# Optimization experiments

Measured on AMD Instinct MI355X. Metric: run time of the kernel, lower is better.

The kernel has to match this reference:

```python
import jax, jax.numpy as jnp
import numpy as np

NUM_HEADS = 16
TEMPERATURE = 1.0


def setup_inputs() -> dict:
    key = jax.random.key(0)
    ks = jax.random.split(key, 6)
    B, H = 2048, 2048
    return {
        "hidden_states": jax.random.normal(ks[0], (B, H), dtype=jnp.float32),
        "attention_mask": jnp.ones((B,), dtype=bool),
        "Wq": jax.random.normal(ks[1], (H, H), dtype=jnp.float32) * 0.02,
        "Wk": jax.random.normal(ks[2], (H, H), dtype=jnp.float32) * 0.02,
        "Wv": jax.random.normal(ks[3], (H, H), dtype=jnp.float32) * 0.02,
        "Wo": jax.random.normal(ks[4], (H, H), dtype=jnp.float32) * 0.02,
        "scale_param": jnp.full((1,), -3.0, dtype=jnp.float32),
    }


def reference(hidden_states, attention_mask, Wq, Wk, Wv, Wo, scale_param):
    B, H = hidden_states.shape
    nh = NUM_HEADS
    hd = H // nh
    # projections (torch Linear: x @ W.T), reshape to [heads, batch, head_dim]
    q = (hidden_states @ Wq.T).reshape(B, nh, hd).transpose(1, 0, 2)
    k = (hidden_states @ Wk.T).reshape(B, nh, hd).transpose(1, 0, 2)
    v = (hidden_states @ Wv.T).reshape(B, nh, hd).transpose(1, 0, 2)
    # cross-batch scores [heads, B, B]
    scores = jnp.einsum('hqd,hkd->hqk', q, k) / (hd ** 0.5 * TEMPERATURE)
    neg_inf = jnp.float32(-jnp.inf)
    eye = jnp.eye(B, dtype=bool)  # exclude self-attention (diagonal)
    scores = jnp.where(eye[None, :, :], neg_inf, scores)
    scores = jnp.where(attention_mask[None, None, :], scores, neg_inf)
    attn = jax.nn.softmax(scores, axis=-1)
    attn = jnp.nan_to_num(attn, nan=0.0)  # rows fully masked -> 0 (dropout=0 is identity)
    ctx = jnp.einsum('hqk,hkd->hqd', attn, v)  # [heads, B, head_dim]
    ctx = ctx.transpose(1, 0, 2).reshape(B, H)
    cross = ctx @ Wo.T
    scale = jax.nn.sigmoid(scale_param[0])
    return hidden_states + scale * cross
```

## Files before the change

kernel.cpp:

```cpp
#include <hip/hip_runtime.h>

typedef __bf16 bf16;
typedef __attribute__((ext_vector_type(8))) __bf16 bf16x8;
typedef __attribute__((ext_vector_type(4))) float f32x4;
typedef __attribute__((ext_vector_type(4))) short s16x4;

#define HDIM 2048

__device__ __forceinline__ void glds16(const void* g, void* l) {
  __builtin_amdgcn_global_load_lds((const __attribute__((address_space(1))) void*)g,
                                   (__attribute__((address_space(3))) void*)l,
                                   16, 0, 0);
}

#define MFMA16(a, b, c) __builtin_amdgcn_mfma_f32_16x16x32_bf16(a, b, c, 0, 0, 0)

__global__ __launch_bounds__(256) void cvt5(
    const float* __restrict__ s0, const float* __restrict__ s1,
    const float* __restrict__ s2, const float* __restrict__ s3,
    const float* __restrict__ s4,
    bf16* __restrict__ d0, bf16* __restrict__ d1, bf16* __restrict__ d2,
    bf16* __restrict__ d3, bf16* __restrict__ d4) {
  const float* s; bf16* d;
  switch (blockIdx.y) {
    case 0: s = s0; d = d0; break;
    case 1: s = s1; d = d1; break;
    case 2: s = s2; d = d2; break;
    case 3: s = s3; d = d3; break;
    default: s = s4; d = d4; break;
  }
  const size_t base = (size_t)blockIdx.x * 4096 + (threadIdx.x << 2);
  for (int i = 0; i < 4; i++) {
    const float4 v = *(const float4*)(s + base + i * 1024);
    union { bf16 h[4]; s16x4 s4v; } u;
    u.h[0] = (bf16)v.x; u.h[1] = (bf16)v.y; u.h[2] = (bf16)v.z; u.h[3] = (bf16)v.w;
    *(s16x4*)(d + base + i * 1024) = u.s4v;
  }
}

__device__ __forceinline__ void gemm128_core(const bf16* __restrict__ A,
                                             const bf16* __restrict__ B,
                                             int rowBase, int colBase,
                                             f32x4 acc[4][4],
                                             bf16* ldsA, bf16* ldsB) {
  const int t = threadIdx.x;
  const int w = t >> 6, l = t & 63;
  const int wr = (w >> 1) << 6, wc = (w & 1) << 6;
  const int lr = l & 15, lq = l >> 4;

  for (int mi = 0; mi < 4; mi++)
    for (int ni = 0; ni < 4; ni++)
      for (int r = 0; r < 4; r++) acc[mi][ni][r] = 0.f;

  const int sRow = (w << 4) + (l >> 2);
  const int sCol = (l & 3) << 3;
  const bf16* gA = A + (size_t)(rowBase + sRow) * HDIM + sCol;
  const bf16* gB = B + (size_t)(colBase + sRow) * HDIM + sCol;
  bf16* lA = ldsA + (w << 9);
  bf16* lB = ldsB + (w << 9);

  for (int k0 = 0; k0 < HDIM; k0 += 32) {
    glds16(gA, lA);
    glds16(gA + (size_t)64 * HDIM, lA + 2048);
    glds16(gB, lB);
    glds16(gB + (size_t)64 * HDIM, lB + 2048);
    gA += 32; gB += 32;
    __syncthreads();

    bf16x8 af[4], bfr[4];
    for (int mi = 0; mi < 4; mi++)
      af[mi] = *(const bf16x8*)&ldsA[(wr + mi * 16 + lr) * 32 + lq * 8];
    for (int ni = 0; ni < 4; ni++)
      bfr[ni] = *(const bf16x8*)&ldsB[(wc + ni * 16 + lr) * 32 + lq * 8];
    for (int mi = 0; mi < 4; mi++)
      for (int ni = 0; ni < 4; ni++)
        acc[mi][ni] = MFMA16(af[mi], bfr[ni], acc[mi][ni]);
    __syncthreads();
  }
}

__global__ __launch_bounds__(256) void qkv_gemm(
    const bf16* __restrict__ hs, const bf16* __restrict__ Wq,
    const bf16* __restrict__ Wk, const bf16* __restrict__ Wv,
    bf16* __restrict__ qb, bf16* __restrict__ Kf, bf16* __restrict__ Vf) {
  __shared__ bf16 ldsA[128 * 32];
  __shared__ bf16 ldsB[128 * 32];
  const int z = blockIdx.z;
  const bf16* W = (z == 0) ? Wq : (z == 1) ? Wk : Wv;
  const int rowBase = blockIdx.y << 7, colBase = blockIdx.x << 7;
  f32x4 acc[4][4];
  gemm128_core(hs, W, rowBase, colBase, acc, ldsA, ldsB);

  const int t = threadIdx.x;
  const int w = t >> 6, l = t & 63;
  const int wr = (w >> 1) << 6, wc = (w & 1) << 6;
  const int lr = l & 15, lq = l >> 4;

  if (z == 0) {
    for (int mi = 0; mi < 4; mi++)
      for (int ni = 0; ni < 4; ni++) {
        const int col = colBase + wc + ni * 16 + lr;
        const int row0 = rowBase + wr + mi * 16 + lq * 4;
        for (int r = 0; r < 4; r++)
          qb[(size_t)(row0 + r) * HDIM + col] = (bf16)acc[mi][ni][r];
      }
  } else if (z == 1) {
    for (int mi = 0; mi < 4; mi++)
      for (int ni = 0; ni < 4; ni++) {
        const int dim = colBase + wc + ni * 16 + lr;
        const int hh = dim >> 7, ks = (dim >> 5) & 3, kh = (dim >> 3) & 3, j = dim & 7;
        const int row0 = rowBase + wr + mi * 16 + lq * 4;
        for (int r = 0; r < 4; r++) {
          const int key = row0 + r;
          const int kbk = key >> 7, kni = (key >> 4) & 7, kl = key & 15;
          Kf[(((size_t)hh * 16 + kbk) * 32 + kni * 4 + ks) * 512 +
             (kh * 16 + kl) * 8 + j] = (bf16)acc[mi][ni][r];
        }
      }
  } else {
    for (int mi = 0; mi < 4; mi++)
      for (int ni = 0; ni < 4; ni++) {
        const int dim = colBase + wc + ni * 16 + lr;
        const int hh = dim >> 7, vni = (dim >> 4) & 7, ll = dim & 15;
        const int row0 = rowBase + wr + mi * 16 + lq * 4;
        const int kbk = row0 >> 7, ks = (row0 >> 5) & 3, lh = (row0 >> 3) & 3;
        const int j0 = row0 & 7;
        union { bf16 h4[4]; s16x4 v; } u;
        for (int r = 0; r < 4; r++) u.h4[r] = (bf16)acc[mi][ni][r];
        *(s16x4*)&Vf[(((size_t)hh * 16 + kbk) * 32 + vni * 4 + ks) * 512 +
                     (lh * 16 + ll) * 8 + j0] = u.v;
      }
  }
}

__global__ __launch_bounds__(512, 2) void attn_kernel(
    const bf16* __restrict__ qb, const bf16* __restrict__ Kf,
    const bf16* __restrict__ Vf, const unsigned char* __restrict__ amask,
    float* __restrict__ Of, float* __restrict__ lsumBuf) {
  __shared__ bf16 Kl[2][32 * 512];
  __shared__ bf16 Vl[2][32 * 512];
  __shared__ bf16 Pl[8 * 32 * 64];

  const int qt = blockIdx.x, h = blockIdx.y, kk = blockIdx.z;
  const int t = threadIdx.x, w = t >> 6, l = t & 63;
  const int lr = l & 15, lq = l >> 4;
  bf16* Pw = Pl + (w << 11);

  bf16x8 aq[2][4];
  for (int mi = 0; mi < 2; mi++)
    for (int ks = 0; ks < 4; ks++)
      aq[mi][ks] = *(const bf16x8*)&qb[(size_t)(qt * 256 + w * 32 + mi * 16 + lr) * HDIM +
                                       h * 128 + ks * 32 + lq * 8];

  f32x4 o[2][8];
  for (int mi = 0; mi < 2; mi++)
    for (int ni = 0; ni < 8; ni++)
      for (int r = 0; r < 4; r++) o[mi][ni][r] = 0.f;
  float lsum[2][4];
  for (int mi = 0; mi < 2; mi++)
    for (int r = 0; r < 4; r++) lsum[mi][r] = 0.f;

  const float c = 0.08838834764831845f * 1.4426950408889634f;

  const size_t headOff = (size_t)h * 16 * 32 * 512;
  const int diagTile = qt * 2 + (w >> 2);

  {
    const size_t t0 = headOff + (size_t)(kk * 8) * 32 * 512;
    for (int i = 0; i < 4; i++) {
      const int frag = i * 8 + w;
      glds16(Kf + t0 + frag * 512 + l * 8, &Kl[0][frag * 512]);
    }
    for (int i = 0; i < 4; i++) {
      const int frag = i * 8 + w;
      glds16(Vf + t0 + frag * 512 + l * 8, &Vl[0][frag * 512]);
    }
  }

  for (int tt = 0; tt < 8; tt++) {
    const int kbk = kk * 8 + tt;
    const int buf = tt & 1;

    __syncthreads();

    if (tt < 7) {
      const size_t tN = headOff + (size_t)(kbk + 1) * 32 * 512;
      for (int i = 0; i < 4; i++) {
        const int frag = i * 8 + w;
        glds16(Kf + tN + frag * 512 + l * 8, &Kl[buf ^ 1][frag * 512]);
      }
      for (int i = 0; i < 4; i++) {
        const int frag = i * 8 + w;
        glds16(Vf + tN + frag * 512 + l * 8, &Vl[buf ^ 1][frag * 512]);
      }
    }

    for (int half = 0; half < 2; half++) {
      f32x4 s[2][4];
      for (int mi = 0; mi < 2; mi++)
        for (int ni = 0; ni < 4; ni++)
          for (int r = 0; r < 4; r++) s[mi][ni][r] = 0.f;
      for (int ks = 0; ks < 4; ks++) {
        bf16x8 bk[4];
        for (int ni = 0; ni < 4; ni++)
          bk[ni] = *(const bf16x8*)&Kl[buf][((half * 4 + ni) * 4 + ks) * 512 + l * 8];
        for (int ni = 0; ni < 4; ni++) {
          s[0][ni] = MFMA16(aq[0][ks], bk[ni], s[0][ni]);
          s[1][ni] = MFMA16(aq[1][ks], bk[ni], s[1][ni]);
        }
      }

      float am[4];
      for (int ni = 0; ni < 4; ni++)
        am[ni] = amask[kbk * 128 + half * 64 + ni * 16 + lr] ? 0.f : -1e30f;
      if (kbk == diagTile) {
        for (int mi = 0; mi < 2; mi++)
          for (int ni = 0; ni < 4; ni++) {
            const int colL = half * 64 + ni * 16 + lr;
            for (int r = 0; r < 4; r++) {
              const int rowL = (w & 3) * 32 + mi * 16 + lq * 4 + r;
              float p = __builtin_exp2f(s[mi][ni][r] * c + am[ni]);
              if (colL == rowL) p = 0.f;
              s[mi][ni][r] = p;
              lsum[mi][r] += p;
            }
          }
      } else {
        for (int mi = 0; mi < 2; mi++)
          for (int ni = 0; ni < 4; ni++)
            for (int r = 0; r < 4; r++) {
              const float p = __builtin_exp2f(s[mi][ni][r] * c + am[ni]);
              s[mi][ni][r] = p;
              lsum[mi][r] += p;
            }
      }

      for (int mi = 0; mi < 2; mi++)
        for (int ni = 0; ni < 4; ni++)
          for (int r = 0; r < 4; r++) {
            const int rl = lq * 4 + r;
            Pw[(mi * 16 + rl) * 64 + (((ni * 2 + (lr >> 3)) ^ (rl & 7)) << 3) +
               (lr & 7)] = (bf16)s[mi][ni][r];
          }

      for (int ksp = 0; ksp < 2; ksp++) {
        bf16x8 bv[8];
        for (int ni = 0; ni < 8; ni++)
          bv[ni] = *(const bf16x8*)&Vl[buf][(ni * 4 + half * 2 + ksp) * 512 + l * 8];
        const int rchunk = ((ksp * 4 + lq) ^ (lr & 7)) << 3;
        const bf16x8 ap0 = *(const bf16x8*)&Pw[lr * 64 + rchunk];
        const bf16x8 ap1 = *(const bf16x8*)&Pw[(16 + lr) * 64 + rchunk];
        for (int ni = 0; ni < 8; ni++) {
          o[0][ni] = MFMA16(ap0, bv[ni], o[0][ni]);
          o[1][ni] = MFMA16(ap1, bv[ni], o[1][ni]);
        }
      }
    }
  }

  for (int mi = 0; mi < 2; mi++)
    for (int r = 0; r < 4; r++)
      for (int off = 1; off < 16; off <<= 1)
        lsum[mi][r] += __shfl_xor(lsum[mi][r], off);

  const size_t obase = (size_t)kk * ((size_t)HDIM * HDIM);
  for (int mi = 0; mi < 2; mi++)
    for (int ni = 0; ni < 8; ni++)
      for (int r = 0; r < 4; r++) {
        const int row = qt * 256 + w * 32 + mi * 16 + lq * 4 + r;
        const int col = h * 128 + ni * 16 + lr;
        Of[obase + (size_t)row * HDIM + col] = o[mi][ni][r];
      }
  if (lr == 0)
    for (int mi = 0; mi < 2; mi++)
      for (int r = 0; r < 4; r++) {
        const int row = qt * 256 + w * 32 + mi * 16 + lq * 4 + r;
        lsumBuf[((size_t)kk * 16 + h) * 2048 + row] = lsum[mi][r];
      }
}

__global__ __launch_bounds__(256) void combine_kernel(
    const float* __restrict__ Of, const float* __restrict__ lsumBuf,
    bf16* __restrict__ ctx) {
  const size_t base = (size_t)blockIdx.x * 2048 + ((size_t)threadIdx.x << 3);
  const int row = (int)(base >> 11);
  const int h = ((int)base & 2047) >> 7;
  const float lt = lsumBuf[h * 2048 + row] + lsumBuf[(16 + h) * 2048 + row];
  const float linv = (lt > 0.f) ? 1.f / lt : 0.f;
  const float* p0 = Of + base;
  const float* p1 = Of + (size_t)4194304 + base;
  const float4 a0 = *(const float4*)p0;
  const float4 a1 = *(const float4*)(p0 + 4);
  const float4 b0 = *(const float4*)p1;
  const float4 b1 = *(const float4*)(p1 + 4);
  union { bf16 hh[8]; s16x4 v[2]; } u;
  u.hh[0] = (bf16)((a0.x + b0.x) * linv);
  u.hh[1] = (bf16)((a0.y + b0.y) * linv);
  u.hh[2] = (bf16)((a0.z + b0.z) * linv);
  u.hh[3] = (bf16)((a0.w + b0.w) * linv);
  u.hh[4] = (bf16)((a1.x + b1.x) * linv);
  u.hh[5] = (bf16)((a1.y + b1.y) * linv);
  u.hh[6] = (bf16)((a1.z + b1.z) * linv);
  u.hh[7] = (bf16)((a1.w + b1.w) * linv);
  *(s16x4*)(ctx + base) = u.v[0];
  *(s16x4*)(ctx + base + 4) = u.v[1];
}

__global__ __launch_bounds__(256) void out_gemm(
    const bf16* __restrict__ ctx, const bf16* __restrict__ Wo,
    const float* __restrict__ hs, const float* __restrict__ scale_p,
    float* __restrict__ outp) {
  __shared__ bf16 ldsA[128 * 32];
  __shared__ bf16 ldsB[64 * 32];
  const int rowBase = blockIdx.y << 7, colBase = blockIdx.x << 6;
  const int t = threadIdx.x;
  const int w = t >> 6, l = t & 63;
  const int wr = (w >> 1) << 6, wc = (w & 1) << 5;
  const int lr = l & 15, lq = l >> 4;

  f32x4 acc[4][2];
  for (int mi = 0; mi < 4; mi++)
    for (int ni = 0; ni < 2; ni++)
      for (int r = 0; r < 4; r++) acc[mi][ni][r] = 0.f;

  const int sRow = (w << 4) + (l >> 2);
  const int sCol = (l & 3) << 3;
  const bf16* gA = ctx + (size_t)(rowBase + sRow) * HDIM + sCol;
  const bf16* gB = Wo + (size_t)(colBase + sRow) * HDIM + sCol;
  bf16* lA = ldsA + (w << 9);
  bf16* lB = ldsB + (w << 9);

  for (int k0 = 0; k0 < HDIM; k0 += 32) {
    glds16(gA, lA);
    glds16(gA + (size_t)64 * HDIM, lA + 2048);
    glds16(gB, lB);
    gA += 32; gB += 32;
    __syncthreads();

    bf16x8 af[4], bfr[2];
    for (int mi = 0; mi < 4; mi++)
      af[mi] = *(const bf16x8*)&ldsA[(wr + mi * 16 + lr) * 32 + lq * 8];
    for (int ni = 0; ni < 2; ni++)
      bfr[ni] = *(const bf16x8*)&ldsB[(wc + ni * 16 + lr) * 32 + lq * 8];
    for (int mi = 0; mi < 4; mi++)
      for (int ni = 0; ni < 2; ni++)
        acc[mi][ni] = MFMA16(af[mi], bfr[ni], acc[mi][ni]);
    __syncthreads();
  }

  const float sig = 1.0f / (1.0f + __expf(-scale_p[0]));
  for (int mi = 0; mi < 4; mi++)
    for (int ni = 0; ni < 2; ni++) {
      const int col = colBase + wc + ni * 16 + lr;
      const int row0 = rowBase + wr + mi * 16 + lq * 4;
      for (int r = 0; r < 4; r++) {
        const size_t idx = (size_t)(row0 + r) * HDIM + col;
        outp[idx] = hs[idx] + sig * acc[mi][ni][r];
      }
    }
}

extern "C" void kernel_launch(void* const* d_in, const int* in_sizes, int n_in,
                              void* d_out, int out_size, void* d_ws, size_t ws_size,
                              hipStream_t stream) {
  const float* hs = (const float*)d_in[0];
  const unsigned char* amask = (const unsigned char*)d_in[1];
  const float* Wq = (const float*)d_in[2];
  const float* Wk = (const float*)d_in[3];
  const float* Wv = (const float*)d_in[4];
  const float* Wo = (const float*)d_in[5];
  const float* scale_p = (const float*)d_in[6];
  float* outp = (float*)d_out;

  const size_t N = (size_t)HDIM * HDIM;
  bf16* qb   = (bf16*)d_ws;
  bf16* Kf   = qb + N;
  bf16* Vf   = Kf + N;
  bf16* ctx  = Vf + N;
  bf16* hs16 = ctx + N;
  bf16* Wq16 = hs16 + N;
  bf16* Wk16 = Wq16 + N;
  bf16* Wv16 = Wk16 + N;
  bf16* Wo16 = Wv16 + N;
  float* Of = (float*)hs16;
  float* lsumBuf = (float*)d_out;

  cvt5<<<dim3(1024, 5), 256, 0, stream>>>(hs, Wq, Wk, Wv, Wo,
                                          hs16, Wq16, Wk16, Wv16, Wo16);
  qkv_gemm<<<dim3(16, 16, 3), 256, 0, stream>>>(hs16, Wq16, Wk16, Wv16, qb, Kf, Vf);
  attn_kernel<<<dim3(8, 16, 2), 512, 0, stream>>>(qb, Kf, Vf, amask, Of, lsumBuf);
  combine_kernel<<<dim3(2048), 256, 0, stream>>>(Of, lsumBuf, ctx);
  out_gemm<<<dim3(32, 16), 256, 0, stream>>>(ctx, Wo16, hs, scale_p, outp);
}
```

Baseline: 275.8 us.

## Double GEMM K-tile to 64 and XOR-swizzle LDS layout in projection GEMMs

```diff
diff --git a/kernel.cpp b/kernel.cpp
--- a/kernel.cpp
+++ b/kernel.cpp
@@ -52,29 +52,32 @@
     for (int ni = 0; ni < 4; ni++)
       for (int r = 0; r < 4; r++) acc[mi][ni][r] = 0.f;
 
-  const int sRow = (w << 4) + (l >> 2);
-  const int sCol = (l & 3) << 3;
-  const bf16* gA = A + (size_t)(rowBase + sRow) * HDIM + sCol;
-  const bf16* gB = B + (size_t)(colBase + sRow) * HDIM + sCol;
-  bf16* lA = ldsA + (w << 9);
-  bf16* lB = ldsB + (w << 9);
-
-  for (int k0 = 0; k0 < HDIM; k0 += 32) {
-    glds16(gA, lA);
-    glds16(gA + (size_t)64 * HDIM, lA + 2048);
-    glds16(gB, lB);
-    glds16(gB + (size_t)64 * HDIM, lB + 2048);
-    gA += 32; gB += 32;
+  const int sRow = l >> 3;
+  const int sCol = ((l & 7) ^ (l >> 3)) << 3;
+  const bf16* gA = A + (size_t)(rowBase + w * 32 + sRow) * HDIM + sCol;
+  const bf16* gB = B + (size_t)(colBase + w * 32 + sRow) * HDIM + sCol;
+  bf16* lA = ldsA + (w << 11);
+  bf16* lB = ldsB + (w << 11);
+
+  for (int k0 = 0; k0 < HDIM; k0 += 64) {
+    for (int i = 0; i < 4; i++) {
+      glds16(gA + (size_t)(i * 8) * HDIM, lA + i * 512);
+      glds16(gB + (size_t)(i * 8) * HDIM, lB + i * 512);
+    }
+    gA += 64; gB += 64;
     __syncthreads();
 
-    bf16x8 af[4], bfr[4];
-    for (int mi = 0; mi < 4; mi++)
-      af[mi] = *(const bf16x8*)&ldsA[(wr + mi * 16 + lr) * 32 + lq * 8];
-    for (int ni = 0; ni < 4; ni++)
-      bfr[ni] = *(const bf16x8*)&ldsB[(wc + ni * 16 + lr) * 32 + lq * 8];
-    for (int mi = 0; mi < 4; mi++)
+    for (int kk = 0; kk < 2; kk++) {
+      const int rs = ((kk * 4 + lq) ^ (lr & 7)) << 3;
+      bf16x8 af[4], bfr[4];
+      for (int mi = 0; mi < 4; mi++)
+        af[mi] = *(const bf16x8*)&ldsA[(wr + mi * 16 + lr) * 64 + rs];
       for (int ni = 0; ni < 4; ni++)
-        acc[mi][ni] = MFMA16(af[mi], bfr[ni], acc[mi][ni]);
+        bfr[ni] = *(const bf16x8*)&ldsB[(wc + ni * 16 + lr) * 64 + rs];
+      for (int mi = 0; mi < 4; mi++)
+        for (int ni = 0; ni < 4; ni++)
+          acc[mi][ni] = MFMA16(af[mi], bfr[ni], acc[mi][ni]);
+    }
     __syncthreads();
   }
 }
@@ -83,8 +86,8 @@
     const bf16* __restrict__ hs, const bf16* __restrict__ Wq,
     const bf16* __restrict__ Wk, const bf16* __restrict__ Wv,
     bf16* __restrict__ qb, bf16* __restrict__ Kf, bf16* __restrict__ Vf) {
-  __shared__ bf16 ldsA[128 * 32];
-  __shared__ bf16 ldsB[128 * 32];
+  __shared__ bf16 ldsA[128 * 64];
+  __shared__ bf16 ldsB[128 * 64];
   const int z = blockIdx.z;
   const bf16* W = (z == 0) ? Wq : (z == 1) ? Wk : Wv;
   const int rowBase = blockIdx.y << 7, colBase = blockIdx.x << 7;
@@ -310,8 +313,8 @@
     const bf16* __restrict__ ctx, const bf16* __restrict__ Wo,
     const float* __restrict__ hs, const float* __restrict__ scale_p,
     float* __restrict__ outp) {
-  __shared__ bf16 ldsA[128 * 32];
-  __shared__ bf16 ldsB[64 * 32];
+  __shared__ bf16 ldsA[128 * 64];
+  __shared__ bf16 ldsB[64 * 64];
   const int rowBase = blockIdx.y << 7, colBase = blockIdx.x << 6;
   const int t = threadIdx.x;
   const int w = t >> 6, l = t & 63;
@@ -323,28 +326,32 @@
     for (int ni = 0; ni < 2; ni++)
       for (int r = 0; r < 4; r++) acc[mi][ni][r] = 0.f;
 
-  const int sRow = (w << 4) + (l >> 2);
-  const int sCol = (l & 3) << 3;
-  const bf16* gA = ctx + (size_t)(rowBase + sRow) * HDIM + sCol;
-  const bf16* gB = Wo + (size_t)(colBase + sRow) * HDIM + sCol;
-  bf16* lA = ldsA + (w << 9);
-  bf16* lB = ldsB + (w << 9);
-
-  for (int k0 = 0; k0 < HDIM; k0 += 32) {
-    glds16(gA, lA);
-    glds16(gA + (size_t)64 * HDIM, lA + 2048);
-    glds16(gB, lB);
-    gA += 32; gB += 32;
+  const int sRow = l >> 3;
+  const int sCol = ((l & 7) ^ (l >> 3)) << 3;
+  const bf16* gA = ctx + (size_t)(rowBase + w * 32 + sRow) * HDIM + sCol;
+  const bf16* gB = Wo + (size_t)(colBase + w * 16 + sRow) * HDIM + sCol;
+  bf16* lA = ldsA + (w << 11);
+  bf16* lB = ldsB + (w << 10);
+
+  for (int k0 = 0; k0 < HDIM; k0 += 64) {
+    for (int i = 0; i < 4; i++)
+      glds16(gA + (size_t)(i * 8) * HDIM, lA + i * 512);
+    for (int i = 0; i < 2; i++)
+      glds16(gB + (size_t)(i * 8) * HDIM, lB + i * 512);
+    gA += 64; gB += 64;
     __syncthreads();
 
-    bf16x8 af[4], bfr[2];
-    for (int mi = 0; mi < 4; mi++)
-      af[mi] = *(const bf16x8*)&ldsA[(wr + mi * 16 + lr) * 32 + lq * 8];
-    for (int ni = 0; ni < 2; ni++)
-      bfr[ni] = *(const bf16x8*)&ldsB[(wc + ni * 16 + lr) * 32 + lq * 8];
-    for (int mi = 0; mi < 4; mi++)
+    for (int kk = 0; kk < 2; kk++) {
+      const int rs = ((kk * 4 + lq) ^ (lr & 7)) << 3;
+      bf16x8 af[4], bfr[2];
+      for (int mi = 0; mi < 4; mi++)
+        af[mi] = *(const bf16x8*)&ldsA[(wr + mi * 16 + lr) * 64 + rs];
       for (int ni = 0; ni < 2; ni++)
-        acc[mi][ni] = MFMA16(af[mi], bfr[ni], acc[mi][ni]);
+        bfr[ni] = *(const bf16x8*)&ldsB[(wc + ni * 16 + lr) * 64 + rs];
+      for (int mi = 0; mi < 4; mi++)
+        for (int ni = 0; ni < 2; ni++)
+          acc[mi][ni] = MFMA16(af[mi], bfr[ni], acc[mi][ni]);
+    }
     __syncthreads();
   }
 
```

Result: no change. 280.3 us (+1.6%).

## Fuse Q/K/V projections into one 768-thread block sharing the A tile

Applied to the files above, without the earlier changes.

```diff
diff --git a/kernel.cpp b/kernel.cpp
--- a/kernel.cpp
+++ b/kernel.cpp
@@ -38,65 +38,57 @@
   }
 }
 
-__device__ __forceinline__ void gemm128_core(const bf16* __restrict__ A,
-                                             const bf16* __restrict__ B,
-                                             int rowBase, int colBase,
-                                             f32x4 acc[4][4],
-                                             bf16* ldsA, bf16* ldsB) {
-  const int t = threadIdx.x;
-  const int w = t >> 6, l = t & 63;
-  const int wr = (w >> 1) << 6, wc = (w & 1) << 6;
-  const int lr = l & 15, lq = l >> 4;
-
-  for (int mi = 0; mi < 4; mi++)
-    for (int ni = 0; ni < 4; ni++)
-      for (int r = 0; r < 4; r++) acc[mi][ni][r] = 0.f;
-
-  const int sRow = (w << 4) + (l >> 2);
-  const int sCol = (l & 3) << 3;
-  const bf16* gA = A + (size_t)(rowBase + sRow) * HDIM + sCol;
-  const bf16* gB = B + (size_t)(colBase + sRow) * HDIM + sCol;
-  bf16* lA = ldsA + (w << 9);
-  bf16* lB = ldsB + (w << 9);
-
-  for (int k0 = 0; k0 < HDIM; k0 += 32) {
-    glds16(gA, lA);
-    glds16(gA + (size_t)64 * HDIM, lA + 2048);
-    glds16(gB, lB);
-    glds16(gB + (size_t)64 * HDIM, lB + 2048);
-    gA += 32; gB += 32;
-    __syncthreads();
-
-    bf16x8 af[4], bfr[4];
-    for (int mi = 0; mi < 4; mi++)
-      af[mi] = *(const bf16x8*)&ldsA[(wr + mi * 16 + lr) * 32 + lq * 8];
-    for (int ni = 0; ni < 4; ni++)
-      bfr[ni] = *(const bf16x8*)&ldsB[(wc + ni * 16 + lr) * 32 + lq * 8];
-    for (int mi = 0; mi < 4; mi++)
-      for (int ni = 0; ni < 4; ni++)
-        acc[mi][ni] = MFMA16(af[mi], bfr[ni], acc[mi][ni]);
-    __syncthreads();
-  }
-}
-
-__global__ __launch_bounds__(256) void qkv_gemm(
+__global__ __launch_bounds__(768, 3) void qkv_gemm(
     const bf16* __restrict__ hs, const bf16* __restrict__ Wq,
     const bf16* __restrict__ Wk, const bf16* __restrict__ Wv,
     bf16* __restrict__ qb, bf16* __restrict__ Kf, bf16* __restrict__ Vf) {
   __shared__ bf16 ldsA[128 * 32];
-  __shared__ bf16 ldsB[128 * 32];
-  const int z = blockIdx.z;
-  const bf16* W = (z == 0) ? Wq : (z == 1) ? Wk : Wv;
+  __shared__ bf16 ldsB[3][128 * 32];
   const int rowBase = blockIdx.y << 7, colBase = blockIdx.x << 7;
+  const int t = threadIdx.x;
+  const int w = t >> 6;
+  const int g = w >> 2;
+  const int wg = w & 3;
+  const int l = t & 63;
+  const int wr = (wg >> 1) << 6, wc = (wg & 1) << 6;
+  const int lr = l & 15, lq = l >> 4;
+
+  const bf16* W = (g == 0) ? Wq : (g == 1) ? Wk : Wv;
+
   f32x4 acc[4][4];
-  gemm128_core(hs, W, rowBase, colBase, acc, ldsA, ldsB);
-
-  const int t = threadIdx.x;
-  const int w = t >> 6, l = t & 63;
-  const int wr = (w >> 1) << 6, wc = (w & 1) << 6;
-  const int lr = l & 15, lq = l >> 4;
-
-  if (z == 0) {
+  for (int mi = 0; mi < 4; mi++)
+    for (int ni = 0; ni < 4; ni++)
+      for (int r = 0; r < 4; r++) acc[mi][ni][r] = 0.f;
+
+  const int sRow = (wg << 4) + (l >> 2);
+  const int sCol = (l & 3) << 3;
+  const bf16* gA = hs + (size_t)(rowBase + sRow) * HDIM + sCol;
+  const bf16* gB = W + (size_t)(colBase + sRow) * HDIM + sCol;
+  bf16* lA = ldsA + (wg << 9);
+  bf16* lB = &ldsB[g][wg << 9];
+
+  for (int k0 = 0; k0 < HDIM; k0 += 32) {
+    if (g == 0) {
+      glds16(gA, lA);
+      glds16(gA + (size_t)64 * HDIM, lA + 2048);
+    }
+    glds16(gB, lB);
+    glds16(gB + (size_t)64 * HDIM, lB + 2048);
+    gA += 32; gB += 32;
+    __syncthreads();
+
+    bf16x8 af[4], bfr[4];
+    for (int mi = 0; mi < 4; mi++)
+      af[mi] = *(const bf16x8*)&ldsA[(wr + mi * 16 + lr) * 32 + lq * 8];
+    for (int ni = 0; ni < 4; ni++)
+      bfr[ni] = *(const bf16x8*)&ldsB[g][(wc + ni * 16 + lr) * 32 + lq * 8];
+    for (int mi = 0; mi < 4; mi++)
+      for (int ni = 0; ni < 4; ni++)
+        acc[mi][ni] = MFMA16(af[mi], bfr[ni], acc[mi][ni]);
+    __syncthreads();
+  }
+
+  if (g == 0) {
     for (int mi = 0; mi < 4; mi++)
       for (int ni = 0; ni < 4; ni++) {
         const int col = colBase + wc + ni * 16 + lr;
@@ -104,7 +96,7 @@
         for (int r = 0; r < 4; r++)
           qb[(size_t)(row0 + r) * HDIM + col] = (bf16)acc[mi][ni][r];
       }
-  } else if (z == 1) {
+  } else if (g == 1) {
     for (int mi = 0; mi < 4; mi++)
       for (int ni = 0; ni < 4; ni++) {
         const int dim = colBase + wc + ni * 16 + lr;
@@ -387,7 +379,7 @@
 
   cvt5<<<dim3(1024, 5), 256, 0, stream>>>(hs, Wq, Wk, Wv, Wo,
                                           hs16, Wq16, Wk16, Wv16, Wo16);
-  qkv_gemm<<<dim3(16, 16, 3), 256, 0, stream>>>(hs16, Wq16, Wk16, Wv16, qb, Kf, Vf);
+  qkv_gemm<<<dim3(16, 16), 768, 0, stream>>>(hs16, Wq16, Wk16, Wv16, qb, Kf, Vf);
   attn_kernel<<<dim3(8, 16, 2), 512, 0, stream>>>(qb, Kf, Vf, amask, Of, lsumBuf);
   combine_kernel<<<dim3(2048), 256, 0, stream>>>(Of, lsumBuf, ctx);
   out_gemm<<<dim3(32, 16), 256, 0, stream>>>(ctx, Wo16, hs, scale_p, outp);
```

Result: slower. 301.9 us (+9.5%).
